# Kernel optimization log

Hardware: AMD Instinct MI355X
Metric: run time of the kernel (lower is better)

The kernel has to match this reference:

```python
import jax, jax.numpy as jnp
import numpy as np

EXPERT_NUM = 8
SEQ_LEN = 2048
FREQ_LEN = SEQ_LEN // 2 + 1
B, C = 32, 512


def setup_inputs() -> dict:
    key = jax.random.key(0)
    k1, k2, k3 = jax.random.split(key, 3)
    x = jax.random.normal(k1, (B, C, SEQ_LEN), dtype=jnp.float32)
    band_boundaries = jax.random.uniform(k2, (EXPERT_NUM - 1,), dtype=jnp.float32)
    gate_w = jax.random.normal(k3, (EXPERT_NUM, FREQ_LEN), dtype=jnp.float32) / np.sqrt(FREQ_LEN)
    gate_b = jnp.zeros((EXPERT_NUM,), dtype=jnp.float32)
    return {"x": x, "band_boundaries": band_boundaries, "gate_w": gate_w, "gate_b": gate_b}


def reference(x, band_boundaries, gate_w, gate_b):
    # x: [B, C, L].  Normalize across channels per (batch, time) position.
    xp = jnp.transpose(x, (0, 2, 1))                       # [B, L, C]
    x_mean = jnp.mean(xp, axis=2, keepdims=True)           # [B, L, 1]
    xc = xp - x_mean
    x_var = jnp.var(xc, axis=2, keepdims=True, ddof=1) + 1e-5  # unbiased, as torch.var
    xn = xc / jnp.sqrt(x_var)
    x_norm = jnp.transpose(xn, (0, 2, 1))                  # [B, C, L]

    freq_x = jnp.fft.rfft(x_norm, axis=-1)                 # [B, C, F] complex
    F = FREQ_LEN

    # Learnable band boundaries -> integer bin boundaries per expert.
    b = jnp.sort(jax.nn.sigmoid(band_boundaries))
    b = jnp.concatenate([jnp.zeros((1,), b.dtype), b, jnp.ones((1,), b.dtype)])
    idx = (b * F).astype(jnp.int32)
    idx = idx.at[-1].set(F)                                # [E+1]

    # Per-frequency-bin expert membership: [E, F] 0/1 mask.
    f = jnp.arange(F)
    member = ((f[None, :] >= idx[:-1, None]) & (f[None, :] < idx[1:, None])).astype(x.dtype)

    # Gating over mean spectral magnitude.
    gating_input = jnp.abs(freq_x).mean(axis=1)            # [B, F]
    gating_scores = jax.nn.softmax(gating_input @ gate_w.T + gate_b, axis=-1)  # [B, E]

    # Fused: per-bin gate weight = sum_e g[b,e] * member[e,f] (no E copies of freq_x).
    w = gating_scores @ member                             # [B, F]
    combined_freq = freq_x * w[:, None, :].astype(freq_x.dtype)

    combined = jnp.fft.irfft(combined_freq, n=SEQ_LEN, axis=-1)  # [B, C, L]

    # De-normalize.
    cp = jnp.transpose(combined, (0, 2, 1))                # [B, L, C]
    out = cp * jnp.sqrt(x_var) + x_mean
    return jnp.transpose(out, (0, 2, 1))                   # [B, C, L]
```

## Files before the change

### kernel.cpp

```cpp
#include <hip/hip_runtime.h>
#include <math.h>

#define NB 32
#define NC 512
#define NF 1025

#define WS_MEAN 0
#define WS_SSTD 65536
#define WS_RSTD 131072
#define WS_GACC 196608
#define WS_WGT  229408
#define WS_PART 262208
#define WS_END_SPLIT (262208 + 262144)
#define WS_SPEC WS_END_SPLIT
#define WS_SPEC_FLOATS (NB * NC * 2048)
#define WS_END_CACHE (WS_SPEC + WS_SPEC_FLOATS)
#define WS_GPART WS_END_CACHE
#define WS_GPART_FLOATS (NB * 64 * NF)
#define WS_END_GPART (WS_GPART + WS_GPART_FLOATS)

#define PIDX(a) ((a) + ((a) >> 4))

__device__ __forceinline__ void stage4(const float* __restrict__ sr,
                                       const float* __restrict__ si,
                                       float* __restrict__ dr,
                                       float* __restrict__ di,
                                       const int ls, const float w1c, const float w1s,
                                       const bool fwd) {
  const int t = threadIdx.x;
  const int s = 1 << ls;
  const int q = t & (s - 1);
  const int p = t >> ls;
  __syncthreads();
  const float ar = sr[PIDX(t)],       ai = si[PIDX(t)];
  const float br = sr[PIDX(t + 256)], bi = si[PIDX(t + 256)];
  const float cr = sr[PIDX(t + 512)], ci = si[PIDX(t + 512)];
  const float er = sr[PIDX(t + 768)], ei = si[PIDX(t + 768)];
  const float apcr = ar + cr, apci = ai + ci;
  const float amcr = ar - cr, amci = ai - ci;
  const float bpdr = br + er, bpdi = bi + ei;
  const float bmdr = br - er, bmdi = bi - ei;
  const float w2r = w1c * w1c - w1s * w1s, w2i = 2.0f * w1c * w1s;
  const float w3r = w2r * w1c - w2i * w1s, w3i = w2r * w1s + w2i * w1c;
  float u1r, u1i, u3r, u3i;
  if (fwd) {
    u1r = amcr + bmdi; u1i = amci - bmdr;
    u3r = amcr - bmdi; u3i = amci + bmdr;
  } else {
    u1r = amcr - bmdi; u1i = amci + bmdr;
    u3r = amcr + bmdi; u3i = amci - bmdr;
  }
  const float x0r = apcr + bpdr, x0i = apci + bpdi;
  const float v2r = apcr - bpdr, v2i = apci - bpdi;
  const float x1r = w1c * u1r - w1s * u1i, x1i = w1c * u1i + w1s * u1r;
  const float x2r = w2r * v2r - w2i * v2i, x2i = w2r * v2i + w2i * v2r;
  const float x3r = w3r * u3r - w3i * u3i, x3i = w3r * u3i + w3i * u3r;
  const int base = q + ((p << 2) << ls);
  dr[PIDX(base)] = x0r;             di[PIDX(base)] = x0i;
  dr[PIDX(base + s)] = x1r;         di[PIDX(base + s)] = x1i;
  dr[PIDX(base + 2 * s)] = x2r;     di[PIDX(base + 2 * s)] = x2i;
  dr[PIDX(base + 3 * s)] = x3r;     di[PIDX(base + 3 * s)] = x3i;
}

__device__ __forceinline__ void stage0_reg(const float2 z0, const float2 z1,
                                           const float2 z2, const float2 z3,
                                           float* __restrict__ dr, float* __restrict__ di,
                                           const float w1c, const float w1s,
                                           const bool fwd) {
  const int t = threadIdx.x;
  const float apcr = z0.x + z2.x, apci = z0.y + z2.y;
  const float amcr = z0.x - z2.x, amci = z0.y - z2.y;
  const float bpdr = z1.x + z3.x, bpdi = z1.y + z3.y;
  const float bmdr = z1.x - z3.x, bmdi = z1.y - z3.y;
  const float w2r = w1c * w1c - w1s * w1s, w2i = 2.0f * w1c * w1s;
  const float w3r = w2r * w1c - w2i * w1s, w3i = w2r * w1s + w2i * w1c;
  float u1r, u1i, u3r, u3i;
  if (fwd) {
    u1r = amcr + bmdi; u1i = amci - bmdr;
    u3r = amcr - bmdi; u3i = amci + bmdr;
  } else {
    u1r = amcr - bmdi; u1i = amci + bmdr;
    u3r = amcr + bmdi; u3i = amci - bmdr;
  }
  const float x0r = apcr + bpdr, x0i = apci + bpdi;
  const float v2r = apcr - bpdr, v2i = apci - bpdi;
  const float x1r = w1c * u1r - w1s * u1i, x1i = w1c * u1i + w1s * u1r;
  const float x2r = w2r * v2r - w2i * v2i, x2i = w2r * v2i + w2i * v2r;
  const float x3r = w3r * u3r - w3i * u3i, x3i = w3r * u3i + w3i * u3r;
  const int base = t << 2;
  dr[PIDX(base)] = x0r;         di[PIDX(base)] = x0i;
  dr[PIDX(base + 1)] = x1r;     di[PIDX(base + 1)] = x1i;
  dr[PIDX(base + 2)] = x2r;     di[PIDX(base + 2)] = x2i;
  dr[PIDX(base + 3)] = x3r;     di[PIDX(base + 3)] = x3i;
}

__device__ __forceinline__ void stage_nt_reg(const float* __restrict__ sr,
                                             const float* __restrict__ si,
                                             float2& o0, float2& o1, float2& o2, float2& o3,
                                             const bool fwd) {
  const int t = threadIdx.x;
  __syncthreads();
  const float ar = sr[PIDX(t)],       ai = si[PIDX(t)];
  const float br = sr[PIDX(t + 256)], bi = si[PIDX(t + 256)];
  const float cr = sr[PIDX(t + 512)], ci = si[PIDX(t + 512)];
  const float er = sr[PIDX(t + 768)], ei = si[PIDX(t + 768)];
  const float apcr = ar + cr, apci = ai + ci;
  const float amcr = ar - cr, amci = ai - ci;
  const float bpdr = br + er, bpdi = bi + ei;
  const float bmdr = br - er, bmdi = bi - ei;
  float u1r, u1i, u3r, u3i;
  if (fwd) {
    u1r = amcr + bmdi; u1i = amci - bmdr;
    u3r = amcr - bmdi; u3i = amci + bmdr;
  } else {
    u1r = amcr - bmdi; u1i = amci + bmdr;
    u3r = amcr + bmdi; u3i = amci - bmdr;
  }
  o0.x = apcr + bpdr;  o0.y = apci + bpdi;
  o1.x = u1r;          o1.y = u1i;
  o2.x = apcr - bpdr;  o2.y = apci - bpdi;
  o3.x = u3r;          o3.y = u3i;
}

__device__ __forceinline__ void fft_twiddles(int t, float& c0, float& s0,
                                             float& c1, float& s1,
                                             float& c2, float& s2,
                                             float& c3, float& s3) {
  __sincosf(-0.00613592315f * (float)t, &s0, &c0);
  __sincosf(-0.02454369261f * (float)(t >> 2), &s1, &c1);
  __sincosf(-0.09817477042f * (float)(t >> 4), &s2, &c2);
  __sincosf(-0.39269908170f * (float)(t >> 6), &s3, &c3);
}

__global__ __launch_bounds__(256) void kmoments(const float* __restrict__ x,
                                                float* __restrict__ ws) {
  const int b = blockIdx.x >> 3;
  const int l = ((blockIdx.x & 7) << 8) + threadIdx.x;
  const float* px = x + (size_t)b * (NC * 2048) + l;
  float sum = 0.f, sq = 0.f;
#pragma unroll 16
  for (int c = 0; c < NC; ++c) {
    float v = px[(size_t)c * 2048];
    sum += v;
    sq = fmaf(v, v, sq);
  }
  float mean = sum * (1.0f / 512.0f);
  float var = fmaf(-512.0f * mean, mean, sq) * (1.0f / 511.0f) + 1e-5f;
  float ss = sqrtf(var);
  int o = (b << 11) + l;
  ws[WS_MEAN + o] = mean;
  ws[WS_SSTD + o] = ss;
  ws[WS_RSTD + o] = 1.0f / ss;
}

__global__ __launch_bounds__(256) void kmoments_part(const float* __restrict__ x,
                                                     float* __restrict__ ws) {
  const int b = blockIdx.x >> 3;
  const int l = ((blockIdx.x & 7) << 8) + threadIdx.x;
  const int half = blockIdx.y;
  const float* px = x + (size_t)b * (NC * 2048) + (size_t)(half * 256) * 2048 + l;
  float sum = 0.f, sq = 0.f;
#pragma unroll 16
  for (int c = 0; c < 256; ++c) {
    float v = px[(size_t)c * 2048];
    sum += v;
    sq = fmaf(v, v, sq);
  }
  int o = (b << 11) + l;
  float2* part = (float2*)(ws + WS_PART) + (half << 16) + o;
  float2 pv; pv.x = sum; pv.y = sq;
  *part = pv;
}

__global__ __launch_bounds__(256) void kmoments_fin(float* __restrict__ ws) {
  const int o = blockIdx.x * 256 + threadIdx.x;
  const float2* part = (const float2*)(ws + WS_PART);
  float2 p0 = part[o];
  float2 p1 = part[(1 << 16) + o];
  float sum = p0.x + p1.x, sq = p0.y + p1.y;
  float mean = sum * (1.0f / 512.0f);
  float var = fmaf(-512.0f * mean, mean, sq) * (1.0f / 511.0f) + 1e-5f;
  float ss = sqrtf(var);
  ws[WS_MEAN + o] = mean;
  ws[WS_SSTD + o] = ss;
  ws[WS_RSTD + o] = 1.0f / ss;
}

__global__ __launch_bounds__(256) void kspec(const float* __restrict__ x,
                                             float* __restrict__ ws,
                                             float2* __restrict__ zout,
                                             float* __restrict__ gpart) {
  __shared__ float Ar[1088], Ai[1088], Br[1088], Bi[1088];
  const int tid = threadIdx.x;
  const int b = blockIdx.x >> 6;
  const int c0 = (blockIdx.x & 63) << 3;
  const float2* mean2 = (const float2*)(ws + WS_MEAN) + ((size_t)b << 10);
  const float2* rstd2 = (const float2*)(ws + WS_RSTD) + ((size_t)b << 10);
  float2 mv[4], rv[4];
#pragma unroll
  for (int j = 0; j < 4; ++j) {
    mv[j] = mean2[tid + (j << 8)];
    rv[j] = rstd2[tid + (j << 8)];
  }
  float w1s, w1c, w2s, w2c;
  __sincosf(-0.00306796158f * (float)tid, &w1s, &w1c);
  __sincosf(-0.00306796158f * (float)(tid + 256), &w2s, &w2c);
  float c0t, s0t, c1t, s1t, c2t, s2t, c3t, s3t;
  fft_twiddles(tid, c0t, s0t, c1t, s1t, c2t, s2t, c3t, s3t);
  float acc0 = 0.f, acc1 = 0.f, acc2 = 0.f, acc3 = 0.f, acc4 = 0.f;
  const float2* xrow = (const float2*)x + ((size_t)(b * NC + c0) << 10);
  float2 v[4];
#pragma unroll
  for (int j = 0; j < 4; ++j) v[j] = xrow[tid + (j << 8)];
  for (int r = 0; r < 8; ++r) {
    float2 zz[4];
#pragma unroll
    for (int j = 0; j < 4; ++j) {
      zz[j].x = (v[j].x - mv[j].x) * rv[j].x;
      zz[j].y = (v[j].y - mv[j].y) * rv[j].y;
    }
    if (r < 7) {
      const float2* nx = xrow + ((size_t)(r + 1) << 10);
#pragma unroll
      for (int j = 0; j < 4; ++j) v[j] = nx[tid + (j << 8)];
    }
    __syncthreads();
    stage0_reg(zz[0], zz[1], zz[2], zz[3], Br, Bi, c0t, s0t, true);
    stage4(Br, Bi, Ar, Ai, 2, c1t, s1t, true);
    stage4(Ar, Ai, Br, Bi, 4, c2t, s2t, true);
    stage4(Br, Bi, Ar, Ai, 6, c3t, s3t, true);
    float2 o0, o1, o2, o3;
    stage_nt_reg(Ar, Ai, o0, o1, o2, o3, true);
    Br[PIDX(tid)] = o0.x;        Bi[PIDX(tid)] = o0.y;
    Br[PIDX(tid + 256)] = o1.x;  Bi[PIDX(tid + 256)] = o1.y;
    Br[PIDX(tid + 512)] = o2.x;  Bi[PIDX(tid + 512)] = o2.y;
    Br[PIDX(tid + 768)] = o3.x;  Bi[PIDX(tid + 768)] = o3.y;
    __syncthreads();
    if (zout) {
      float2* zrow = zout + ((size_t)(b * NC + c0 + r) << 10);
      zrow[tid] = o0;
      zrow[tid + 256] = o1;
      zrow[tid + 512] = o2;
      zrow[tid + 768] = o3;
    }
    if (tid == 0) {
      float zr = Br[PIDX(0)], zi = Bi[PIDX(0)];
      acc0 += fabsf(zr + zi);
      acc1 += fabsf(zr - zi);
      float mr = Br[PIDX(512)], mi = Bi[PIDX(512)];
      acc4 += sqrtf(mr * mr + mi * mi);
    } else {
      const int k = tid;
      float zkr = Br[PIDX(k)], zki = Bi[PIDX(k)];
      float zmr = Br[PIDX(1024 - k)], zmi = Bi[PIDX(1024 - k)];
      float Ar_ = 0.5f * (zkr + zmr), Ai_ = 0.5f * (zki - zmi);
      float Br_ = 0.5f * (zki + zmi), Bi_ = -0.5f * (zkr - zmr);
      float WBr = Br_ * w1c - Bi_ * w1s, WBi = Br_ * w1s + Bi_ * w1c;
      float Xr = Ar_ + WBr, Xi = Ai_ + WBi;
      float Yr = Ar_ - WBr, Yi = Ai_ - WBi;
      acc0 += sqrtf(Xr * Xr + Xi * Xi);
      acc1 += sqrtf(Yr * Yr + Yi * Yi);
    }
    {
      const int k = tid + 256;
      float zkr = Br[PIDX(k)], zki = Bi[PIDX(k)];
      float zmr = Br[PIDX(1024 - k)], zmi = Bi[PIDX(1024 - k)];
      float Ar_ = 0.5f * (zkr + zmr), Ai_ = 0.5f * (zki - zmi);
      float Br_ = 0.5f * (zki + zmi), Bi_ = -0.5f * (zkr - zmr);
      float WBr = Br_ * w2c - Bi_ * w2s, WBi = Br_ * w2s + Bi_ * w2c;
      float Xr = Ar_ + WBr, Xi = Ai_ + WBi;
      float Yr = Ar_ - WBr, Yi = Ai_ - WBi;
      acc2 += sqrtf(Xr * Xr + Xi * Xi);
      acc3 += sqrtf(Yr * Yr + Yi * Yi);
    }
  }
  if (gpart) {
    float* prow = gpart + (size_t)blockIdx.x * NF;
    prow[tid] = acc0;
    prow[1024 - tid] = acc1;
    prow[tid + 256] = acc2;
    prow[768 - tid] = acc3;
    if (tid == 0) prow[512] = acc4;
  } else {
    float* g = ws + WS_GACC + b * NF;
    atomicAdd(g + tid, acc0);
    atomicAdd(g + 1024 - tid, acc1);
    atomicAdd(g + tid + 256, acc2);
    atomicAdd(g + 768 - tid, acc3);
    if (tid == 0) atomicAdd(g + 512, acc4);
  }
}

__global__ __launch_bounds__(256) void kgate(float* __restrict__ ws,
                                             const float* __restrict__ gw,
                                             const float* __restrict__ gb,
                                             const float* __restrict__ bb,
                                             const float* __restrict__ gpart) {
  const float* gacc = ws + WS_GACC;
  float* wgt = ws + WS_WGT;
  const int b = blockIdx.x;
  const int tid = threadIdx.x;
  __shared__ float red[256];
  __shared__ float sc[8];
  __shared__ int sidx[9];
  float acc[8];
#pragma unroll
  for (int e = 0; e < 8; ++e) acc[e] = 0.f;
  for (int f = tid; f < NF; f += 256) {
    float g;
    if (gpart) {
      const float* gp = gpart + (size_t)b * 64 * NF + f;
      g = 0.f;
#pragma unroll 8
      for (int j = 0; j < 64; ++j) g += gp[j * NF];
    } else {
      g = gacc[b * NF + f];
    }
    g *= (1.0f / 512.0f);
#pragma unroll
    for (int e = 0; e < 8; ++e) acc[e] = fmaf(g, gw[e * NF + f], acc[e]);
  }
#pragma unroll
  for (int e = 0; e < 8; ++e) {
    __syncthreads();
    red[tid] = acc[e];
    __syncthreads();
    for (int s2 = 128; s2 > 0; s2 >>= 1) {
      if (tid < s2) red[tid] += red[tid + s2];
      __syncthreads();
    }
    if (tid == 0) sc[e] = red[0] + gb[e];
  }
  __syncthreads();
  if (tid == 0) {
    float mx = sc[0];
    for (int e = 1; e < 8; ++e) mx = fmaxf(mx, sc[e]);
    float sum = 0.f;
    float ex[8];
    for (int e = 0; e < 8; ++e) { ex[e] = expf(sc[e] - mx); sum += ex[e]; }
    for (int e = 0; e < 8; ++e) sc[e] = ex[e] / sum;
    float sv[7];
    for (int i2 = 0; i2 < 7; ++i2) sv[i2] = 1.0f / (1.0f + expf(-bb[i2]));
    for (int i2 = 1; i2 < 7; ++i2) {
      float key = sv[i2];
      int j2 = i2 - 1;
      while (j2 >= 0 && sv[j2] > key) { sv[j2 + 1] = sv[j2]; --j2; }
      sv[j2 + 1] = key;
    }
    sidx[0] = 0;
    for (int i2 = 0; i2 < 7; ++i2) sidx[i2 + 1] = (int)(sv[i2] * 1025.0f);
    sidx[8] = 1025;
  }
  __syncthreads();
  for (int f = tid; f < NF; f += 256) {
    float wv = 0.f;
#pragma unroll
    for (int e = 0; e < 8; ++e)
      if (f >= sidx[e] && f < sidx[e + 1]) wv += sc[e];
    wgt[b * NF + f] = wv;
  }
}

__device__ __forceinline__ void combine_pair(float* __restrict__ zr_, float* __restrict__ zi_,
                                             int k, float wc, float ws_, float wk, float wmk) {
  const int ik = PIDX(k), im = PIDX(1024 - k);
  float zkr = zr_[ik], zki = zi_[ik];
  float zmr = zr_[im], zmi = zi_[im];
  float Ar_ = 0.5f * (zkr + zmr), Ai_ = 0.5f * (zki - zmi);
  float Br2 = 0.5f * (zki + zmi), Bi2 = -0.5f * (zkr - zmr);
  float WBr = Br2 * wc - Bi2 * ws_, WBi = Br2 * ws_ + Bi2 * wc;
  float Xr = Ar_ + WBr, Xi = Ai_ + WBi;
  float Xcr = Ar_ - WBr, Xci = Ai_ - WBi;
  float XpR = wk * Xr, XpI = wk * Xi;
  float XcpR = wmk * Xcr, XcpI = wmk * Xci;
  float Apr = 0.5f * (XpR + XcpR), Api = 0.5f * (XpI + XcpI);
  float Er = 0.5f * (XpR - XcpR), Ei = 0.5f * (XpI - XcpI);
  float Bpr = Er * wc + Ei * ws_;
  float Bpi = Ei * wc - Er * ws_;
  zr_[ik] = Apr - Bpi;  zi_[ik] = Api + Bpr;
  zr_[im] = Apr + Bpi;  zi_[im] = Bpr - Api;
}

__global__ __launch_bounds__(256) void kapply(const float* __restrict__ x,
                                              float* __restrict__ out,
                                              const float* __restrict__ ws) {
  __shared__ float Ar[1088], Ai[1088], Br[1088], Bi[1088];
  const int tid = threadIdx.x;
  const int b = blockIdx.x >> 9;
  const float2* mean2 = (const float2*)(ws + WS_MEAN) + ((size_t)b << 10);
  const float2* sstd2 = (const float2*)(ws + WS_SSTD) + ((size_t)b << 10);
  const float2* rstd2 = (const float2*)(ws + WS_RSTD) + ((size_t)b << 10);
  const float2* x2 = (const float2*)x + ((size_t)blockIdx.x << 10);
  const float* wrow = ws + WS_WGT + b * NF;
  float wk1 = wrow[tid];
  float wm1 = wrow[1024 - tid];
  float wk2 = wrow[tid + 256];
  float wm2 = wrow[768 - tid];
  float wmid = wrow[512];
  float w1s, w1c, w2s, w2c;
  __sincosf(-0.00306796158f * (float)tid, &w1s, &w1c);
  __sincosf(-0.00306796158f * (float)(tid + 256), &w2s, &w2c);
  float c0t, s0t, c1t, s1t, c2t, s2t, c3t, s3t;
  fft_twiddles(tid, c0t, s0t, c1t, s1t, c2t, s2t, c3t, s3t);
  float2 mv[4], rv[4], ssv[4];
#pragma unroll
  for (int j = 0; j < 4; ++j) {
    mv[j] = mean2[tid + (j << 8)];
    rv[j] = rstd2[tid + (j << 8)];
    ssv[j] = sstd2[tid + (j << 8)];
  }
  float2 zz[4];
#pragma unroll
  for (int j = 0; j < 4; ++j) {
    float2 v = x2[tid + (j << 8)];
    zz[j].x = (v.x - mv[j].x) * rv[j].x;
    zz[j].y = (v.y - mv[j].y) * rv[j].y;
  }
  stage0_reg(zz[0], zz[1], zz[2], zz[3], Br, Bi, c0t, s0t, true);
  stage4(Br, Bi, Ar, Ai, 2, c1t, s1t, true);
  stage4(Ar, Ai, Br, Bi, 4, c2t, s2t, true);
  stage4(Br, Bi, Ar, Ai, 6, c3t, s3t, true);
  float2 f0, f1, f2, f3;
  stage_nt_reg(Ar, Ai, f0, f1, f2, f3, true);
  Br[PIDX(tid)] = f0.x;        Bi[PIDX(tid)] = f0.y;
  Br[PIDX(tid + 256)] = f1.x;  Bi[PIDX(tid + 256)] = f1.y;
  Br[PIDX(tid + 512)] = f2.x;  Bi[PIDX(tid + 512)] = f2.y;
  Br[PIDX(tid + 768)] = f3.x;  Bi[PIDX(tid + 768)] = f3.y;
  __syncthreads();
  if (tid == 0) {
    float zr = Br[PIDX(0)], zi = Bi[PIDX(0)];
    float X0 = (zr + zi) * wk1;
    float XM = (zr - zi) * wm1;
    Br[PIDX(0)] = 0.5f * (X0 + XM);
    Bi[PIDX(0)] = 0.5f * (X0 - XM);
    Br[PIDX(512)] *= wmid;
    Bi[PIDX(512)] *= wmid;
  } else {
    combine_pair(Br, Bi, tid, w1c, w1s, wk1, wm1);
  }
  combine_pair(Br, Bi, tid + 256, w2c, w2s, wk2, wm2);
  stage4(Br, Bi, Ar, Ai, 0, c0t, -s0t, false);
  stage4(Ar, Ai, Br, Bi, 2, c1t, -s1t, false);
  stage4(Br, Bi, Ar, Ai, 4, c2t, -s2t, false);
  stage4(Ar, Ai, Br, Bi, 6, c3t, -s3t, false);
  float2 o0, o1, o2, o3;
  stage_nt_reg(Br, Bi, o0, o1, o2, o3, false);
  const float inv = 1.0f / 1024.0f;
  float2* out2 = (float2*)out + ((size_t)blockIdx.x << 10);
  float2 oo;
  oo.x = fmaf(o0.x * inv, ssv[0].x, mv[0].x);
  oo.y = fmaf(o0.y * inv, ssv[0].y, mv[0].y);
  out2[tid] = oo;
  oo.x = fmaf(o1.x * inv, ssv[1].x, mv[1].x);
  oo.y = fmaf(o1.y * inv, ssv[1].y, mv[1].y);
  out2[tid + 256] = oo;
  oo.x = fmaf(o2.x * inv, ssv[2].x, mv[2].x);
  oo.y = fmaf(o2.y * inv, ssv[2].y, mv[2].y);
  out2[tid + 512] = oo;
  oo.x = fmaf(o3.x * inv, ssv[3].x, mv[3].x);
  oo.y = fmaf(o3.y * inv, ssv[3].y, mv[3].y);
  out2[tid + 768] = oo;
}

__global__ __launch_bounds__(256) void kapply_z(const float2* __restrict__ z,
                                                float* __restrict__ out,
                                                const float* __restrict__ ws) {
  __shared__ float Ar[1088], Ai[1088], Br[1088], Bi[1088];
  const int tid = threadIdx.x;
  const int b = blockIdx.x >> 9;
  const float2* mean2 = (const float2*)(ws + WS_MEAN) + ((size_t)b << 10);
  const float2* sstd2 = (const float2*)(ws + WS_SSTD) + ((size_t)b << 10);
  const float* wrow = ws + WS_WGT + b * NF;
  float wk1 = wrow[tid];
  float wm1 = wrow[1024 - tid];
  float wk2 = wrow[tid + 256];
  float wm2 = wrow[768 - tid];
  float wmid = wrow[512];
  float w1s, w1c, w2s, w2c;
  __sincosf(-0.00306796158f * (float)tid, &w1s, &w1c);
  __sincosf(-0.00306796158f * (float)(tid + 256), &w2s, &w2c);
  float c0t, s0t, c1t, s1t, c2t, s2t, c3t, s3t;
  fft_twiddles(tid, c0t, s0t, c1t, s1t, c2t, s2t, c3t, s3t);
  const float2* zrow = z + ((size_t)blockIdx.x << 10);
  float2 mv[4], ssv[4];
#pragma unroll
  for (int j = 0; j < 4; ++j) {
    mv[j] = mean2[tid + (j << 8)];
    ssv[j] = sstd2[tid + (j << 8)];
  }
#pragma unroll
  for (int j = 0; j < 4; ++j) {
    const int n = tid + (j << 8);
    float2 v = zrow[n];
    Br[PIDX(n)] = v.x;
    Bi[PIDX(n)] = v.y;
  }
  __syncthreads();
  if (tid == 0) {
    float zr = Br[PIDX(0)], zi = Bi[PIDX(0)];
    float X0 = (zr + zi) * wk1;
    float XM = (zr - zi) * wm1;
    Br[PIDX(0)] = 0.5f * (X0 + XM);
    Bi[PIDX(0)] = 0.5f * (X0 - XM);
    Br[PIDX(512)] *= wmid;
    Bi[PIDX(512)] *= wmid;
  } else {
    combine_pair(Br, Bi, tid, w1c, w1s, wk1, wm1);
  }
  combine_pair(Br, Bi, tid + 256, w2c, w2s, wk2, wm2);
  stage4(Br, Bi, Ar, Ai, 0, c0t, -s0t, false);
  stage4(Ar, Ai, Br, Bi, 2, c1t, -s1t, false);
  stage4(Br, Bi, Ar, Ai, 4, c2t, -s2t, false);
  stage4(Ar, Ai, Br, Bi, 6, c3t, -s3t, false);
  float2 o0, o1, o2, o3;
  stage_nt_reg(Br, Bi, o0, o1, o2, o3, false);
  const float inv = 1.0f / 1024.0f;
  float2* out2 = (float2*)out + ((size_t)blockIdx.x << 10);
  float2 oo;
  oo.x = fmaf(o0.x * inv, ssv[0].x, mv[0].x);
  oo.y = fmaf(o0.y * inv, ssv[0].y, mv[0].y);
  out2[tid] = oo;
  oo.x = fmaf(o1.x * inv, ssv[1].x, mv[1].x);
  oo.y = fmaf(o1.y * inv, ssv[1].y, mv[1].y);
  out2[tid + 256] = oo;
  oo.x = fmaf(o2.x * inv, ssv[2].x, mv[2].x);
  oo.y = fmaf(o2.y * inv, ssv[2].y, mv[2].y);
  out2[tid + 512] = oo;
  oo.x = fmaf(o3.x * inv, ssv[3].x, mv[3].x);
  oo.y = fmaf(o3.y * inv, ssv[3].y, mv[3].y);
  out2[tid + 768] = oo;
}

extern "C" void kernel_launch(void* const* d_in, const int* in_sizes, int n_in,
                              void* d_out, int out_size, void* d_ws, size_t ws_size,
                              hipStream_t stream) {
  const float* x = (const float*)d_in[0];
  const float* bb = (const float*)d_in[1];
  const float* gw = (const float*)d_in[2];
  const float* gb = (const float*)d_in[3];
  float* ws = (float*)d_ws;
  float* out = (float*)d_out;

  const bool split = ws_size >= (size_t)WS_END_SPLIT * sizeof(float);
  const bool cache = ws_size >= (size_t)WS_END_CACHE * sizeof(float);
  const bool part = ws_size >= (size_t)WS_END_GPART * sizeof(float);

  if (!part) {
    hipMemsetAsync((char*)d_ws + WS_GACC * sizeof(float), 0, (NB * NF) * sizeof(float), stream);
  }
  if (split) {
    kmoments_part<<<dim3(NB * 8, 2), dim3(256), 0, stream>>>(x, ws);
    kmoments_fin<<<dim3(256), dim3(256), 0, stream>>>(ws);
  } else {
    kmoments<<<dim3(NB * 8), dim3(256), 0, stream>>>(x, ws);
  }
  kspec<<<dim3(NB * 64), dim3(256), 0, stream>>>(x, ws,
      cache ? (float2*)(ws + WS_SPEC) : nullptr,
      part ? (ws + WS_GPART) : nullptr);
  kgate<<<dim3(NB), dim3(256), 0, stream>>>(ws, gw, gb, bb,
      part ? (ws + WS_GPART) : nullptr);
  if (cache) {
    kapply_z<<<dim3(NB * NC), dim3(256), 0, stream>>>((const float2*)(ws + WS_SPEC), out, ws);
  } else {
    kapply<<<dim3(NB * NC), dim3(256), 0, stream>>>(x, out, ws);
  }
}
```

Before: 352.1 us.

## Process two FFT rows per barrier in forward and inverse kernels

The forward spectrum kernel and the cached inverse-apply kernel now transform two channel rows together using doubled shared-memory buffers, so each __syncthreads is shared by two independent FFTs. This halves the barrier count per row and gives each thread two independent chains of work to interleave. The inverse kernel launches half as many blocks, each handling two rows. The cost is twice the shared memory per block, which may reduce how many blocks fit on each CU.

```diff
diff --git a/kernel.cpp b/kernel.cpp
--- a/kernel.cpp
+++ b/kernel.cpp
@@ -21,17 +21,16 @@
 
 #define PIDX(a) ((a) + ((a) >> 4))
 
-__device__ __forceinline__ void stage4(const float* __restrict__ sr,
-                                       const float* __restrict__ si,
-                                       float* __restrict__ dr,
-                                       float* __restrict__ di,
-                                       const int ls, const float w1c, const float w1s,
-                                       const bool fwd) {
+__device__ __forceinline__ void stage4_body(const float* __restrict__ sr,
+                                            const float* __restrict__ si,
+                                            float* __restrict__ dr,
+                                            float* __restrict__ di,
+                                            const int ls, const float w1c, const float w1s,
+                                            const bool fwd) {
   const int t = threadIdx.x;
   const int s = 1 << ls;
   const int q = t & (s - 1);
   const int p = t >> ls;
-  __syncthreads();
   const float ar = sr[PIDX(t)],       ai = si[PIDX(t)];
   const float br = sr[PIDX(t + 256)], bi = si[PIDX(t + 256)];
   const float cr = sr[PIDX(t + 512)], ci = si[PIDX(t + 512)];
@@ -60,6 +59,16 @@
   dr[PIDX(base + s)] = x1r;         di[PIDX(base + s)] = x1i;
   dr[PIDX(base + 2 * s)] = x2r;     di[PIDX(base + 2 * s)] = x2i;
   dr[PIDX(base + 3 * s)] = x3r;     di[PIDX(base + 3 * s)] = x3i;
+}
+
+__device__ __forceinline__ void stage4(const float* __restrict__ sr,
+                                       const float* __restrict__ si,
+                                       float* __restrict__ dr,
+                                       float* __restrict__ di,
+                                       const int ls, const float w1c, const float w1s,
+                                       const bool fwd) {
+  __syncthreads();
+  stage4_body(sr, si, dr, di, ls, w1c, w1s, fwd);
 }
 
 __device__ __forceinline__ void stage0_reg(const float2 z0, const float2 z1,
@@ -94,12 +103,11 @@
   dr[PIDX(base + 3)] = x3r;     di[PIDX(base + 3)] = x3i;
 }
 
-__device__ __forceinline__ void stage_nt_reg(const float* __restrict__ sr,
-                                             const float* __restrict__ si,
-                                             float2& o0, float2& o1, float2& o2, float2& o3,
-                                             const bool fwd) {
+__device__ __forceinline__ void stage_nt_body(const float* __restrict__ sr,
+                                              const float* __restrict__ si,
+                                              float2& o0, float2& o1, float2& o2, float2& o3,
+                                              const bool fwd) {
   const int t = threadIdx.x;
-  __syncthreads();
   const float ar = sr[PIDX(t)],       ai = si[PIDX(t)];
   const float br = sr[PIDX(t + 256)], bi = si[PIDX(t + 256)];
   const float cr = sr[PIDX(t + 512)], ci = si[PIDX(t + 512)];
@@ -122,6 +130,14 @@
   o3.x = u3r;          o3.y = u3i;
 }
 
+__device__ __forceinline__ void stage_nt_reg(const float* __restrict__ sr,
+                                             const float* __restrict__ si,
+                                             float2& o0, float2& o1, float2& o2, float2& o3,
+                                             const bool fwd) {
+  __syncthreads();
+  stage_nt_body(sr, si, o0, o1, o2, o3, fwd);
+}
+
 __device__ __forceinline__ void fft_twiddles(int t, float& c0, float& s0,
                                              float& c1, float& s1,
                                              float& c2, float& s2,
@@ -130,6 +146,45 @@
   __sincosf(-0.02454369261f * (float)(t >> 2), &s1, &c1);
   __sincosf(-0.09817477042f * (float)(t >> 4), &s2, &c2);
   __sincosf(-0.39269908170f * (float)(t >> 6), &s3, &c3);
+}
+
+__device__ __forceinline__ void mag_accum(const float* __restrict__ Br_,
+                                          const float* __restrict__ Bi_,
+                                          const int tid,
+                                          const float w1c, const float w1s,
+                                          const float w2c, const float w2s,
+                                          float& acc0, float& acc1, float& acc2,
+                                          float& acc3, float& acc4) {
+  if (tid == 0) {
+    float zr = Br_[PIDX(0)], zi = Bi_[PIDX(0)];
+    acc0 += fabsf(zr + zi);
+    acc1 += fabsf(zr - zi);
+    float mr = Br_[PIDX(512)], mi = Bi_[PIDX(512)];
+    acc4 += sqrtf(mr * mr + mi * mi);
+  } else {
+    const int k = tid;
+    float zkr = Br_[PIDX(k)], zki = Bi_[PIDX(k)];
+    float zmr = Br_[PIDX(1024 - k)], zmi = Bi_[PIDX(1024 - k)];
+    float Ar_ = 0.5f * (zkr + zmr), Ai_ = 0.5f * (zki - zmi);
+    float Bq = 0.5f * (zki + zmi), Bi2 = -0.5f * (zkr - zmr);
+    float WBr = Bq * w1c - Bi2 * w1s, WBi = Bq * w1s + Bi2 * w1c;
+    float Xr = Ar_ + WBr, Xi = Ai_ + WBi;
+    float Yr = Ar_ - WBr, Yi = Ai_ - WBi;
+    acc0 += sqrtf(Xr * Xr + Xi * Xi);
+    acc1 += sqrtf(Yr * Yr + Yi * Yi);
+  }
+  {
+    const int k = tid + 256;
+    float zkr = Br_[PIDX(k)], zki = Bi_[PIDX(k)];
+    float zmr = Br_[PIDX(1024 - k)], zmi = Bi_[PIDX(1024 - k)];
+    float Ar_ = 0.5f * (zkr + zmr), Ai_ = 0.5f * (zki - zmi);
+    float Bq = 0.5f * (zki + zmi), Bi2 = -0.5f * (zkr - zmr);
+    float WBr = Bq * w2c - Bi2 * w2s, WBi = Bq * w2s + Bi2 * w2c;
+    float Xr = Ar_ + WBr, Xi = Ai_ + WBi;
+    float Yr = Ar_ - WBr, Yi = Ai_ - WBi;
+    acc2 += sqrtf(Xr * Xr + Xi * Xi);
+    acc3 += sqrtf(Yr * Yr + Yi * Yi);
+  }
 }
 
 __global__ __launch_bounds__(256) void kmoments(const float* __restrict__ x,
@@ -190,7 +245,8 @@
                                              float* __restrict__ ws,
                                              float2* __restrict__ zout,
                                              float* __restrict__ gpart) {
-  __shared__ float Ar[1088], Ai[1088], Br[1088], Bi[1088];
+  __shared__ float A0r[1088], A0i[1088], B0r[1088], B0i[1088];
+  __shared__ float A1r[1088], A1i[1088], B1r[1088], B1i[1088];
   const int tid = threadIdx.x;
   const int b = blockIdx.x >> 6;
   const int c0 = (blockIdx.x & 63) << 3;
@@ -209,70 +265,66 @@
   fft_twiddles(tid, c0t, s0t, c1t, s1t, c2t, s2t, c3t, s3t);
   float acc0 = 0.f, acc1 = 0.f, acc2 = 0.f, acc3 = 0.f, acc4 = 0.f;
   const float2* xrow = (const float2*)x + ((size_t)(b * NC + c0) << 10);
-  float2 v[4];
-#pragma unroll
-  for (int j = 0; j < 4; ++j) v[j] = xrow[tid + (j << 8)];
-  for (int r = 0; r < 8; ++r) {
-    float2 zz[4];
+  float2 v0[4], v1[4];
+#pragma unroll
+  for (int j = 0; j < 4; ++j) {
+    v0[j] = xrow[tid + (j << 8)];
+    v1[j] = xrow[(1 << 10) + tid + (j << 8)];
+  }
+  for (int rp = 0; rp < 4; ++rp) {
+    float2 zz0[4], zz1[4];
 #pragma unroll
     for (int j = 0; j < 4; ++j) {
-      zz[j].x = (v[j].x - mv[j].x) * rv[j].x;
-      zz[j].y = (v[j].y - mv[j].y) * rv[j].y;
+      zz0[j].x = (v0[j].x - mv[j].x) * rv[j].x;
+      zz0[j].y = (v0[j].y - mv[j].y) * rv[j].y;
+      zz1[j].x = (v1[j].x - mv[j].x) * rv[j].x;
+      zz1[j].y = (v1[j].y - mv[j].y) * rv[j].y;
     }
-    if (r < 7) {
-      const float2* nx = xrow + ((size_t)(r + 1) << 10);
-#pragma unroll
-      for (int j = 0; j < 4; ++j) v[j] = nx[tid + (j << 8)];
+    if (rp < 3) {
+      const float2* nx = xrow + ((size_t)(2 * rp + 2) << 10);
+#pragma unroll
+      for (int j = 0; j < 4; ++j) {
+        v0[j] = nx[tid + (j << 8)];
+        v1[j] = nx[(1 << 10) + tid + (j << 8)];
+      }
     }
     __syncthreads();
-    stage0_reg(zz[0], zz[1], zz[2], zz[3], Br, Bi, c0t, s0t, true);
-    stage4(Br, Bi, Ar, Ai, 2, c1t, s1t, true);
-    stage4(Ar, Ai, Br, Bi, 4, c2t, s2t, true);
-    stage4(Br, Bi, Ar, Ai, 6, c3t, s3t, true);
+    stage0_reg(zz0[0], zz0[1], zz0[2], zz0[3], B0r, B0i, c0t, s0t, true);
+    stage0_reg(zz1[0], zz1[1], zz1[2], zz1[3], B1r, B1i, c0t, s0t, true);
+    __syncthreads();
+    stage4_body(B0r, B0i, A0r, A0i, 2, c1t, s1t, true);
+    stage4_body(B1r, B1i, A1r, A1i, 2, c1t, s1t, true);
+    __syncthreads();
+    stage4_body(A0r, A0i, B0r, B0i, 4, c2t, s2t, true);
+    stage4_body(A1r, A1i, B1r, B1i, 4, c2t, s2t, true);
+    __syncthreads();
+    stage4_body(B0r, B0i, A0r, A0i, 6, c3t, s3t, true);
+    stage4_body(B1r, B1i, A1r, A1i, 6, c3t, s3t, true);
+    __syncthreads();
     float2 o0, o1, o2, o3;
-    stage_nt_reg(Ar, Ai, o0, o1, o2, o3, true);
-    Br[PIDX(tid)] = o0.x;        Bi[PIDX(tid)] = o0.y;
-    Br[PIDX(tid + 256)] = o1.x;  Bi[PIDX(tid + 256)] = o1.y;
-    Br[PIDX(tid + 512)] = o2.x;  Bi[PIDX(tid + 512)] = o2.y;
-    Br[PIDX(tid + 768)] = o3.x;  Bi[PIDX(tid + 768)] = o3.y;
-    __syncthreads();
+    stage_nt_body(A0r, A0i, o0, o1, o2, o3, true);
+    B0r[PIDX(tid)] = o0.x;        B0i[PIDX(tid)] = o0.y;
+    B0r[PIDX(tid + 256)] = o1.x;  B0i[PIDX(tid + 256)] = o1.y;
+    B0r[PIDX(tid + 512)] = o2.x;  B0i[PIDX(tid + 512)] = o2.y;
+    B0r[PIDX(tid + 768)] = o3.x;  B0i[PIDX(tid + 768)] = o3.y;
     if (zout) {
-      float2* zrow = zout + ((size_t)(b * NC + c0 + r) << 10);
-      zrow[tid] = o0;
-      zrow[tid + 256] = o1;
-      zrow[tid + 512] = o2;
-      zrow[tid + 768] = o3;
+      float2* zrow = zout + ((size_t)(b * NC + c0 + 2 * rp) << 10);
+      zrow[tid] = o0; zrow[tid + 256] = o1;
+      zrow[tid + 512] = o2; zrow[tid + 768] = o3;
     }
-    if (tid == 0) {
-      float zr = Br[PIDX(0)], zi = Bi[PIDX(0)];
-      acc0 += fabsf(zr + zi);
-      acc1 += fabsf(zr - zi);
-      float mr = Br[PIDX(512)], mi = Bi[PIDX(512)];
-      acc4 += sqrtf(mr * mr + mi * mi);
-    } else {
-      const int k = tid;
-      float zkr = Br[PIDX(k)], zki = Bi[PIDX(k)];
-      float zmr = Br[PIDX(1024 - k)], zmi = Bi[PIDX(1024 - k)];
-      float Ar_ = 0.5f * (zkr + zmr), Ai_ = 0.5f * (zki - zmi);
-      float Br_ = 0.5f * (zki + zmi), Bi_ = -0.5f * (zkr - zmr);
-      float WBr = Br_ * w1c - Bi_ * w1s, WBi = Br_ * w1s + Bi_ * w1c;
-      float Xr = Ar_ + WBr, Xi = Ai_ + WBi;
-      float Yr = Ar_ - WBr, Yi = Ai_ - WBi;
-      acc0 += sqrtf(Xr * Xr + Xi * Xi);
-      acc1 += sqrtf(Yr * Yr + Yi * Yi);
+    stage_nt_body(A1r, A1i, o0, o1, o2, o3, true);
+    B1r[PIDX(tid)] = o0.x;        B1i[PIDX(tid)] = o0.y;
+    B1r[PIDX(tid + 256)] = o1.x;  B1i[PIDX(tid + 256)] = o1.y;
+    B1r[PIDX(tid + 512)] = o2.x;  B1i[PIDX(tid + 512)] = o2.y;
+    B1r[PIDX(tid + 768)] = o3.x;  B1i[PIDX(tid + 768)] = o3.y;
+    if (zout) {
+      float2* zrow = zout + ((size_t)(b * NC + c0 + 2 * rp + 1) << 10);
+      zrow[tid] = o0; zrow[tid + 256] = o1;
+      zrow[tid + 512] = o2; zrow[tid + 768] = o3;
     }
-    {
-      const int k = tid + 256;
-      float zkr = Br[PIDX(k)], zki = Bi[PIDX(k)];
-      float zmr = Br[PIDX(1024 - k)], zmi = Bi[PIDX(1024 - k)];
-      float Ar_ = 0.5f * (zkr + zmr), Ai_ = 0.5f * (zki - zmi);
-      float Br_ = 0.5f * (zki + zmi), Bi_ = -0.5f * (zkr - zmr);
-      float WBr = Br_ * w2c - Bi_ * w2s, WBi = Br_ * w2s + Bi_ * w2c;
-      float Xr = Ar_ + WBr, Xi = Ai_ + WBi;
-      float Yr = Ar_ - WBr, Yi = Ai_ - WBi;
-      acc2 += sqrtf(Xr * Xr + Xi * Xi);
-      acc3 += sqrtf(Yr * Yr + Yi * Yi);
-    }
+    __syncthreads();
+    mag_accum(B0r, B0i, tid, w1c, w1s, w2c, w2s, acc0, acc1, acc2, acc3, acc4);
+    mag_accum(B1r, B1i, tid, w1c, w1s, w2c, w2s, acc0, acc1, acc2, acc3, acc4);
   }
   if (gpart) {
     float* prow = gpart + (size_t)blockIdx.x * NF;
@@ -379,6 +431,27 @@
   float Bpi = Ei * wc - Er * ws_;
   zr_[ik] = Apr - Bpi;  zi_[ik] = Api + Bpr;
   zr_[im] = Apr + Bpi;  zi_[im] = Bpr - Api;
+}
+
+__device__ __forceinline__ void combine_all(float* __restrict__ Br_, float* __restrict__ Bi_,
+                                            const int tid,
+                                            const float w1c, const float w1s,
+                                            const float w2c, const float w2s,
+                                            const float wk1, const float wm1,
+                                            const float wk2, const float wm2,
+                                            const float wmid) {
+  if (tid == 0) {
+    float zr = Br_[PIDX(0)], zi = Bi_[PIDX(0)];
+    float X0 = (zr + zi) * wk1;
+    float XM = (zr - zi) * wm1;
+    Br_[PIDX(0)] = 0.5f * (X0 + XM);
+    Bi_[PIDX(0)] = 0.5f * (X0 - XM);
+    Br_[PIDX(512)] *= wmid;
+    Bi_[PIDX(512)] *= wmid;
+  } else {
+    combine_pair(Br_, Bi_, tid, w1c, w1s, wk1, wm1);
+  }
+  combine_pair(Br_, Bi_, tid + 256, w2c, w2s, wk2, wm2);
 }
 
 __global__ __launch_bounds__(256) void kapply(const float* __restrict__ x,
@@ -427,18 +500,7 @@
   Br[PIDX(tid + 512)] = f2.x;  Bi[PIDX(tid + 512)] = f2.y;
   Br[PIDX(tid + 768)] = f3.x;  Bi[PIDX(tid + 768)] = f3.y;
   __syncthreads();
-  if (tid == 0) {
-    float zr = Br[PIDX(0)], zi = Bi[PIDX(0)];
-    float X0 = (zr + zi) * wk1;
-    float XM = (zr - zi) * wm1;
-    Br[PIDX(0)] = 0.5f * (X0 + XM);
-    Bi[PIDX(0)] = 0.5f * (X0 - XM);
-    Br[PIDX(512)] *= wmid;
-    Bi[PIDX(512)] *= wmid;
-  } else {
-    combine_pair(Br, Bi, tid, w1c, w1s, wk1, wm1);
-  }
-  combine_pair(Br, Bi, tid + 256, w2c, w2s, wk2, wm2);
+  combine_all(Br, Bi, tid, w1c, w1s, w2c, w2s, wk1, wm1, wk2, wm2, wmid);
   stage4(Br, Bi, Ar, Ai, 0, c0t, -s0t, false);
   stage4(Ar, Ai, Br, Bi, 2, c1t, -s1t, false);
   stage4(Br, Bi, Ar, Ai, 4, c2t, -s2t, false);
@@ -465,9 +527,11 @@
 __global__ __launch_bounds__(256) void kapply_z(const float2* __restrict__ z,
                                                 float* __restrict__ out,
                                                 const float* __restrict__ ws) {
-  __shared__ float Ar[1088], Ai[1088], Br[1088], Bi[1088];
+  __shared__ float A0r[1088], A0i[1088], B0r[1088], B0i[1088];
+  __shared__ float A1r[1088], A1i[1088], B1r[1088], B1i[1088];
   const int tid = threadIdx.x;
-  const int b = blockIdx.x >> 9;
+  const int g = blockIdx.x << 1;
+  const int b = g >> 9;
   const float2* mean2 = (const float2*)(ws + WS_MEAN) + ((size_t)b << 10);
   const float2* sstd2 = (const float2*)(ws + WS_SSTD) + ((size_t)b << 10);
   const float* wrow = ws + WS_WGT + b * NF;
@@ -481,7 +545,8 @@
   __sincosf(-0.00306796158f * (float)(tid + 256), &w2s, &w2c);
   float c0t, s0t, c1t, s1t, c2t, s2t, c3t, s3t;
   fft_twiddles(tid, c0t, s0t, c1t, s1t, c2t, s2t, c3t, s3t);
-  const float2* zrow = z + ((size_t)blockIdx.x << 10);
+  const float2* zrow0 = z + ((size_t)g << 10);
+  const float2* zrow1 = z + ((size_t)(g + 1) << 10);
   float2 mv[4], ssv[4];
 #pragma unroll
   for (int j = 0; j < 4; ++j) {
@@ -491,44 +556,57 @@
 #pragma unroll
   for (int j = 0; j < 4; ++j) {
     const int n = tid + (j << 8);
-    float2 v = zrow[n];
-    Br[PIDX(n)] = v.x;
-    Bi[PIDX(n)] = v.y;
-  }
-  __syncthreads();
-  if (tid == 0) {
-    float zr = Br[PIDX(0)], zi = Bi[PIDX(0)];
-    float X0 = (zr + zi) * wk1;
-    float XM = (zr - zi) * wm1;
-    Br[PIDX(0)] = 0.5f * (X0 + XM);
-    Bi[PIDX(0)] = 0.5f * (X0 - XM);
-    Br[PIDX(512)] *= wmid;
-    Bi[PIDX(512)] *= wmid;
-  } else {
-    combine_pair(Br, Bi, tid, w1c, w1s, wk1, wm1);
-  }
-  combine_pair(Br, Bi, tid + 256, w2c, w2s, wk2, wm2);
-  stage4(Br, Bi, Ar, Ai, 0, c0t, -s0t, false);
-  stage4(Ar, Ai, Br, Bi, 2, c1t, -s1t, false);
-  stage4(Br, Bi, Ar, Ai, 4, c2t, -s2t, false);
-  stage4(Ar, Ai, Br, Bi, 6, c3t, -s3t, false);
-  float2 o0, o1, o2, o3;
-  stage_nt_reg(Br, Bi, o0, o1, o2, o3, false);
+    float2 q0 = zrow0[n];
+    float2 q1 = zrow1[n];
+    B0r[PIDX(n)] = q0.x;  B0i[PIDX(n)] = q0.y;
+    B1r[PIDX(n)] = q1.x;  B1i[PIDX(n)] = q1.y;
+  }
+  __syncthreads();
+  combine_all(B0r, B0i, tid, w1c, w1s, w2c, w2s, wk1, wm1, wk2, wm2, wmid);
+  combine_all(B1r, B1i, tid, w1c, w1s, w2c, w2s, wk1, wm1, wk2, wm2, wmid);
+  __syncthreads();
+  stage4_body(B0r, B0i, A0r, A0i, 0, c0t, -s0t, false);
+  stage4_body(B1r, B1i, A1r, A1i, 0, c0t, -s0t, false);
+  __syncthreads();
+  stage4_body(A0r, A0i, B0r, B0i, 2, c1t, -s1t, false);
+  stage4_body(A1r, A1i, B1r, B1i, 2, c1t, -s1t, false);
+  __syncthreads();
+  stage4_body(B0r, B0i, A0r, A0i, 4, c2t, -s2t, false);
+  stage4_body(B1r, B1i, A1r, A1i, 4, c2t, -s2t, false);
+  __syncthreads();
+  stage4_body(A0r, A0i, B0r, B0i, 6, c3t, -s3t, false);
+  stage4_body(A1r, A1i, B1r, B1i, 6, c3t, -s3t, false);
+  __syncthreads();
   const float inv = 1.0f / 1024.0f;
-  float2* out2 = (float2*)out + ((size_t)blockIdx.x << 10);
-  float2 oo;
+  float2 o0, o1, o2, o3, oo;
+  float2* out0 = (float2*)out + ((size_t)g << 10);
+  stage_nt_body(B0r, B0i, o0, o1, o2, o3, false);
   oo.x = fmaf(o0.x * inv, ssv[0].x, mv[0].x);
   oo.y = fmaf(o0.y * inv, ssv[0].y, mv[0].y);
-  out2[tid] = oo;
+  out0[tid] = oo;
   oo.x = fmaf(o1.x * inv, ssv[1].x, mv[1].x);
   oo.y = fmaf(o1.y * inv, ssv[1].y, mv[1].y);
-  out2[tid + 256] = oo;
+  out0[tid + 256] = oo;
   oo.x = fmaf(o2.x * inv, ssv[2].x, mv[2].x);
   oo.y = fmaf(o2.y * inv, ssv[2].y, mv[2].y);
-  out2[tid + 512] = oo;
+  out0[tid + 512] = oo;
   oo.x = fmaf(o3.x * inv, ssv[3].x, mv[3].x);
   oo.y = fmaf(o3.y * inv, ssv[3].y, mv[3].y);
-  out2[tid + 768] = oo;
+  out0[tid + 768] = oo;
+  float2* out1 = (float2*)out + ((size_t)(g + 1) << 10);
+  stage_nt_body(B1r, B1i, o0, o1, o2, o3, false);
+  oo.x = fmaf(o0.x * inv, ssv[0].x, mv[0].x);
+  oo.y = fmaf(o0.y * inv, ssv[0].y, mv[0].y);
+  out1[tid] = oo;
+  oo.x = fmaf(o1.x * inv, ssv[1].x, mv[1].x);
+  oo.y = fmaf(o1.y * inv, ssv[1].y, mv[1].y);
+  out1[tid + 256] = oo;
+  oo.x = fmaf(o2.x * inv, ssv[2].x, mv[2].x);
+  oo.y = fmaf(o2.y * inv, ssv[2].y, mv[2].y);
+  out1[tid + 512] = oo;
+  oo.x = fmaf(o3.x * inv, ssv[3].x, mv[3].x);
+  oo.y = fmaf(o3.y * inv, ssv[3].y, mv[3].y);
+  out1[tid + 768] = oo;
 }
 
 extern "C" void kernel_launch(void* const* d_in, const int* in_sizes, int n_in,
@@ -560,7 +638,7 @@
   kgate<<<dim3(NB), dim3(256), 0, stream>>>(ws, gw, gb, bb,
       part ? (ws + WS_GPART) : nullptr);
   if (cache) {
-    kapply_z<<<dim3(NB * NC), dim3(256), 0, stream>>>((const float2*)(ws + WS_SPEC), out, ws);
+    kapply_z<<<dim3(NB * NC / 2), dim3(256), 0, stream>>>((const float2*)(ws + WS_SPEC), out, ws);
   } else {
     kapply<<<dim3(NB * NC), dim3(256), 0, stream>>>(x, out, ws);
   }
```

Result: slower. 368.5 us (+4.7%).
